# Kernel tuning notes

Hardware: AMD Instinct MI355X
Metric: run time of the kernel (lower is better)

The kernel has to match this reference:

```python
import jax, jax.numpy as jnp
import numpy as np

B, A, NB, BOND = 256, 100, 10, 110
AF, BF, H, DEPTH = 82, 6, 300, 3

def setup_inputs() -> dict:
    key = jax.random.key(0)
    ks = jax.random.split(key, 16)
    atom_feats = jax.random.normal(ks[0], (B, A, AF), dtype=jnp.float32)
    bond_feats = jax.random.normal(ks[1], (B, BOND, BF), dtype=jnp.float32)
    ag_b = jax.random.randint(ks[2], (B, A, NB, 1), 0, B, dtype=jnp.int32)
    ag_a = jax.random.randint(ks[3], (B, A, NB, 1), 0, A, dtype=jnp.int32)
    atom_graph = jnp.concatenate([ag_b, ag_a], axis=-1)
    bg_b = jax.random.randint(ks[4], (B, A, NB, 1), 0, B, dtype=jnp.int32)
    bg_e = jax.random.randint(ks[5], (B, A, NB, 1), 0, BOND, dtype=jnp.int32)
    bond_graph = jnp.concatenate([bg_b, bg_e], axis=-1)
    num_nbs = jax.random.randint(ks[6], (B, A), 0, NB + 1, dtype=jnp.int32)
    n_atoms = jax.random.randint(ks[7], (B,), 50, A + 1, dtype=jnp.int32)
    n_atoms = n_atoms.at[0].set(A)  # padding must equal n_atoms.max()
    sc = lambda i, o: (2.0 / (i + o)) ** 0.5
    w_fc1 = jax.random.normal(ks[8], (AF, H), dtype=jnp.float32) * sc(AF, H)
    w_nei = jax.random.normal(ks[9], (H + BF, H), dtype=jnp.float32) * sc(H + BF, H)
    b_nei = jnp.zeros((H,), dtype=jnp.float32)
    w_atom = jax.random.normal(ks[10], (2 * H, H), dtype=jnp.float32) * sc(2 * H, H)
    b_atom = jnp.zeros((H,), dtype=jnp.float32)
    w2a = jax.random.normal(ks[11], (H, H), dtype=jnp.float32) * sc(H, H)
    w2b = jax.random.normal(ks[12], (BF, H), dtype=jnp.float32) * sc(BF, H)
    w_fc2 = jax.random.normal(ks[13], (H, H), dtype=jnp.float32) * sc(H, H)
    return dict(atom_feats=atom_feats, bond_feats=bond_feats, w_fc1=w_fc1,
                w_nei=w_nei, b_nei=b_nei, w_atom=w_atom, b_atom=b_atom,
                w2a=w2a, w2b=w2b, w_fc2=w_fc2, atom_graph=atom_graph,
                bond_graph=bond_graph, num_nbs=num_nbs, n_atoms=n_atoms)

def reference(atom_feats, bond_feats, w_fc1, w_nei, b_nei, w_atom, b_atom,
              w2a, w2b, w_fc2, atom_graph, bond_graph, num_nbs, n_atoms):
    h = jax.nn.relu(atom_feats @ w_fc1)                      # [B,A,H]
    bondnei = bond_feats[bond_graph[..., 0], bond_graph[..., 1]]  # [B,A,NB,BF]
    mask_neis = (num_nbs[..., None] > jnp.arange(NB, dtype=jnp.int32))[..., None]
    mask_atoms = (n_atoms[:, None] > jnp.arange(A, dtype=jnp.int32))[..., None]
    for i in range(DEPTH):
        atomnei = h[atom_graph[..., 0], atom_graph[..., 1]]  # [B,A,NB,H]
        if i + 1 == DEPTH:
            nei = (atomnei @ w2a) * (bondnei @ w2b)          # [B,A,NB,H]
            nei = jnp.where(mask_neis, nei, 0.0).sum(-2)     # [B,A,H]
            local = (h @ w_fc2) * nei
            local = jnp.where(mask_atoms, local, 0.0)
        else:
            nei = jax.nn.relu(jnp.concatenate([atomnei, bondnei], -1) @ w_nei + b_nei)
            nei = jnp.where(mask_neis, nei, 0.0).sum(-2)
            h = jax.nn.relu(jnp.concatenate([h, nei], -1) @ w_atom + b_atom)
    return local
```

## Files before the change

### kernel.cpp

```cpp
#include <hip/hip_runtime.h>

#define B_    256
#define A_    100
#define NB_   10
#define BOND_ 110
#define AF_   82
#define BF_   6
#define H_    300
#define NP_   320
#define MA_   (B_ * A_)
#define MB_   (B_ * BOND_)
#define KP300 320
#define KP82  96

typedef __attribute__((ext_vector_type(8))) short short8;
typedef __attribute__((ext_vector_type(4))) float f32x4;

__device__ __forceinline__ ushort f2bf(float v) {
    union { float f; unsigned u; } x; x.f = v;
    unsigned r = x.u + 0x7fffu + ((x.u >> 16) & 1u);
    return (ushort)(r >> 16);
}
__device__ __forceinline__ float bf2f(ushort h) {
    union { float f; unsigned u; } x; x.u = ((unsigned)h) << 16;
    return x.f;
}

__device__ __forceinline__ void gload16(const void* g, void* l) {
    __builtin_amdgcn_global_load_lds(
        (const __attribute__((address_space(1))) void*)g,
        (__attribute__((address_space(3))) void*)l, 16, 0, 0);
}

template<bool DUAL, bool BIAS, bool RELU, int OUTMODE>
__global__ __launch_bounds__(256, 2) void mgemm_k(
    const ushort* __restrict__ aH, const ushort* __restrict__ aL,
    const ushort* __restrict__ wH, const ushort* __restrict__ wL,
    const ushort* __restrict__ aH2, const ushort* __restrict__ aL2,
    const ushort* __restrict__ wH2, const ushort* __restrict__ wL2,
    int KP,
    const float* __restrict__ bias,
    const float* __restrict__ E,
    const int*   __restrict__ n_atoms,
    ushort* __restrict__ oHi, ushort* __restrict__ oLo,
    float*  __restrict__ oF)
{
    __shared__ ushort lds[3840 * 8];
    const int tid  = threadIdx.x;
    const int m0   = blockIdx.x * 64;
    const int lane = tid & 63;
    const int l16  = lane & 15;
    const int kg   = lane >> 4;
    const int w    = tid >> 6;

    int sel[15]; int off[15];
    #pragma unroll
    for (int q = 0; q < 15; ++q) {
        int G = q * 256 + tid;
        int s, local;
        if      (G < 320)  { s = 0; local = G; }
        else if (G < 640)  { s = 1; local = G - 320; }
        else if (G < 2240) { s = 2; local = G - 640; }
        else               { s = 3; local = G - 2240; }
        int rc = local / 5;
        int ch = local % 5; if (ch == 4) ch = 3;
        int rowterm = (s < 2) ? (m0 + rc) : rc;
        sel[q] = s;
        off[q] = rowterm * KP * 2 + ch * 16;
    }
    char* ldst = (char*)&lds[0] + ((tid & 192) << 4);

    f32x4 acc[4][5] = {};
    const int aoff = l16 * 80 + kg * 16;
    const int boff = (w * 80 + l16) * 80 + kg * 16;

    const int npass = DUAL ? 2 : 1;
    for (int pass = 0; pass < npass; ++pass) {
        const ushort* s0 = (DUAL && pass) ? aH2 : aH;
        const ushort* s1 = (DUAL && pass) ? aL2 : aL;
        const ushort* s2 = (DUAL && pass) ? wH2 : wH;
        const ushort* s3 = (DUAL && pass) ? wL2 : wL;
        const char* ptr[15];
        #pragma unroll
        for (int q = 0; q < 15; ++q) {
            const ushort* b = (sel[q] == 0) ? s0 : (sel[q] == 1) ? s1 : (sel[q] == 2) ? s2 : s3;
            ptr[q] = (const char*)b + off[q];
        }
        const int ksteps = KP >> 5;
        for (int ks = 0; ks < ksteps; ++ks) {
            __syncthreads();
            #pragma unroll
            for (int q = 0; q < 15; ++q) gload16(ptr[q], ldst + q * 4096);
            __syncthreads();

            short8 ah[4], al[4];
            #pragma unroll
            for (int rt = 0; rt < 4; ++rt) {
                ah[rt] = *(const short8*)((const char*)lds +     0 + aoff + rt * 1280);
                al[rt] = *(const short8*)((const char*)lds +  5120 + aoff + rt * 1280);
            }
            #pragma unroll
            for (int c = 0; c < 5; ++c) {
                short8 bh = *(const short8*)((const char*)lds + 10240 + boff + c * 1280);
                short8 bl = *(const short8*)((const char*)lds + 35840 + boff + c * 1280);
                #pragma unroll
                for (int rt = 0; rt < 4; ++rt) {
                    acc[rt][c] = __builtin_amdgcn_mfma_f32_16x16x32_bf16(ah[rt], bh, acc[rt][c], 0, 0, 0);
                    acc[rt][c] = __builtin_amdgcn_mfma_f32_16x16x32_bf16(al[rt], bh, acc[rt][c], 0, 0, 0);
                    acc[rt][c] = __builtin_amdgcn_mfma_f32_16x16x32_bf16(ah[rt], bl, acc[rt][c], 0, 0, 0);
                }
            }
            #pragma unroll
            for (int q = 0; q < 15; ++q) ptr[q] += 64;
        }
    }

    float biasv[5];
    #pragma unroll
    for (int c = 0; c < 5; ++c) {
        int col = w * 80 + c * 16 + l16;
        biasv[c] = (BIAS && col < H_) ? bias[col] : 0.f;
    }
    #pragma unroll
    for (int rt = 0; rt < 4; ++rt) {
        #pragma unroll
        for (int c = 0; c < 5; ++c) {
            const int col = w * 80 + c * 16 + l16;
            #pragma unroll
            for (int r = 0; r < 4; ++r) {
                const int row = m0 + rt * 16 + kg * 4 + r;
                float v = acc[rt][c][r];
                if (BIAS) v += biasv[c];
                if (RELU) v = fmaxf(v, 0.f);
                if (OUTMODE == 0) {
                    ushort hi = f2bf(v);
                    ushort lo = f2bf(v - bf2f(hi));
                    size_t o = (size_t)row * NP_ + col;
                    oHi[o] = hi; oLo[o] = lo;
                } else if (OUTMODE == 1) {
                    oF[(size_t)row * NP_ + col] = v;
                } else {
                    if (col < H_) {
                        v *= E[(size_t)row * NP_ + col];
                        int b = row / A_;
                        int a = row - b * A_;
                        if (a >= n_atoms[b]) v = 0.f;
                        oF[(size_t)row * H_ + col] = v;
                    }
                }
            }
        }
    }
}

__global__ __launch_bounds__(256) void conv_w_k(
    const float* __restrict__ src, int K, int KP,
    ushort* __restrict__ dhi, ushort* __restrict__ dlo)
{
    int idx = blockIdx.x * 256 + threadIdx.x;
    if (idx >= NP_ * KP) return;
    int c = idx / KP, k = idx - c * KP;
    float v = (c < H_ && k < K) ? src[(size_t)k * H_ + c] : 0.f;
    ushort hi = f2bf(v);
    dhi[idx] = hi;
    dlo[idx] = f2bf(v - bf2f(hi));
}

__global__ __launch_bounds__(256) void conv_af_k(
    const float* __restrict__ src, ushort* __restrict__ dhi, ushort* __restrict__ dlo)
{
    int idx = blockIdx.x * 256 + threadIdx.x;
    if (idx >= MA_ * KP82) return;
    int row = idx / KP82, k = idx - row * KP82;
    float v = (k < AF_) ? src[(size_t)row * AF_ + k] : 0.f;
    ushort hi = f2bf(v);
    dhi[idx] = hi;
    dlo[idx] = f2bf(v - bf2f(hi));
}

__global__ __launch_bounds__(256) void bondmm_k(
    const float* __restrict__ bf, const float* __restrict__ wmat,
    const float* __restrict__ bias, float* __restrict__ out)
{
    int idx = blockIdx.x * 256 + threadIdx.x;
    if (idx >= MB_ * 80) return;
    int row = idx / 80, c4 = idx - row * 80;
    float4 s = make_float4(0.f, 0.f, 0.f, 0.f);
    if (c4 < 75) {
        int col = c4 * 4;
        if (bias) s = *(const float4*)(bias + col);
        #pragma unroll
        for (int k = 0; k < 6; ++k) {
            float b = bf[(size_t)row * 6 + k];
            float4 wv = *(const float4*)(wmat + (size_t)k * H_ + col);
            s.x = fmaf(b, wv.x, s.x); s.y = fmaf(b, wv.y, s.y);
            s.z = fmaf(b, wv.z, s.z); s.w = fmaf(b, wv.w, s.w);
        }
    }
    *(float4*)(out + (size_t)row * NP_ + c4 * 4) = s;
}

__global__ __launch_bounds__(256) void agg_relu_k(
    const float* __restrict__ hw, const float* __restrict__ bwn,
    const int* __restrict__ ag, const int* __restrict__ bg,
    const int* __restrict__ num_nbs,
    ushort* __restrict__ neiH, ushort* __restrict__ neiL)
{
    int idx = blockIdx.x * 256 + threadIdx.x;
    if (idx >= MA_ * 80) return;
    int ba = idx / 80, c4 = idx - ba * 80;
    int nn = num_nbs[ba];
    const int* agp = ag + (size_t)ba * NB_ * 2;
    const int* bgp = bg + (size_t)ba * NB_ * 2;
    float4 s = make_float4(0.f, 0.f, 0.f, 0.f);
    for (int n = 0; n < nn; ++n) {
        int arow = agp[2*n] * A_    + agp[2*n+1];
        int brow = bgp[2*n] * BOND_ + bgp[2*n+1];
        float4 hv = *(const float4*)(hw  + (size_t)arow * NP_ + c4 * 4);
        float4 bv = *(const float4*)(bwn + (size_t)brow * NP_ + c4 * 4);
        s.x += fmaxf(hv.x + bv.x, 0.f); s.y += fmaxf(hv.y + bv.y, 0.f);
        s.z += fmaxf(hv.z + bv.z, 0.f); s.w += fmaxf(hv.w + bv.w, 0.f);
    }
    size_t o = (size_t)ba * NP_ + c4 * 4;
    ushort4 hi, lo;
    hi.x = f2bf(s.x); lo.x = f2bf(s.x - bf2f(hi.x));
    hi.y = f2bf(s.y); lo.y = f2bf(s.y - bf2f(hi.y));
    hi.z = f2bf(s.z); lo.z = f2bf(s.z - bf2f(hi.z));
    hi.w = f2bf(s.w); lo.w = f2bf(s.w - bf2f(hi.w));
    *(ushort4*)(neiH + o) = hi;
    *(ushort4*)(neiL + o) = lo;
}

__global__ __launch_bounds__(256) void agg_prod_k(
    const float* __restrict__ hw2, const float* __restrict__ bw2,
    const int* __restrict__ ag, const int* __restrict__ bg,
    const int* __restrict__ num_nbs, float* __restrict__ neiF)
{
    int idx = blockIdx.x * 256 + threadIdx.x;
    if (idx >= MA_ * 80) return;
    int ba = idx / 80, c4 = idx - ba * 80;
    int nn = num_nbs[ba];
    const int* agp = ag + (size_t)ba * NB_ * 2;
    const int* bgp = bg + (size_t)ba * NB_ * 2;
    float4 s = make_float4(0.f, 0.f, 0.f, 0.f);
    for (int n = 0; n < nn; ++n) {
        int arow = agp[2*n] * A_    + agp[2*n+1];
        int brow = bgp[2*n] * BOND_ + bgp[2*n+1];
        float4 hv = *(const float4*)(hw2 + (size_t)arow * NP_ + c4 * 4);
        float4 bv = *(const float4*)(bw2 + (size_t)brow * NP_ + c4 * 4);
        s.x = fmaf(hv.x, bv.x, s.x); s.y = fmaf(hv.y, bv.y, s.y);
        s.z = fmaf(hv.z, bv.z, s.z); s.w = fmaf(hv.w, bv.w, s.w);
    }
    *(float4*)(neiF + (size_t)ba * NP_ + c4 * 4) = s;
}

extern "C" void kernel_launch(void* const* d_in, const int* in_sizes, int n_in,
                              void* d_out, int out_size, void* d_ws, size_t ws_size,
                              hipStream_t stream)
{
    const float* atom_feats = (const float*)d_in[0];
    const float* bond_feats = (const float*)d_in[1];
    const float* w_fc1      = (const float*)d_in[2];
    const float* w_nei      = (const float*)d_in[3];
    const float* b_nei      = (const float*)d_in[4];
    const float* w_atom     = (const float*)d_in[5];
    const float* b_atom     = (const float*)d_in[6];
    const float* w2a        = (const float*)d_in[7];
    const float* w2b        = (const float*)d_in[8];
    const float* w_fc2      = (const float*)d_in[9];
    const int*   atom_graph = (const int*)d_in[10];
    const int*   bond_graph = (const int*)d_in[11];
    const int*   num_nbs    = (const int*)d_in[12];
    const int*   n_atoms    = (const int*)d_in[13];
    float* out = (float*)d_out;
    (void)in_sizes; (void)n_in; (void)out_size; (void)ws_size;

    const size_t SZ_H16 = (size_t)MA_ * NP_ * 2;
    const size_t SZ_HF  = (size_t)MA_ * NP_ * 4;
    const size_t SZ_BWN = (size_t)MB_ * NP_ * 4;
    const size_t SZ_AF  = (size_t)MA_ * KP82 * 2;
    const size_t SZ_WT  = (size_t)NP_ * KP300 * 2;
    const size_t SZ_WT1 = (size_t)NP_ * KP82 * 2;
    char* p = (char*)d_ws;
    ushort* hA_h = (ushort*)p; p += SZ_H16;
    ushort* hA_l = (ushort*)p; p += SZ_H16;
    ushort* hB_h = (ushort*)p; p += SZ_H16;
    ushort* hB_l = (ushort*)p; p += SZ_H16;
    ushort* nei_h = (ushort*)p; p += SZ_H16;
    ushort* nei_l = (ushort*)p; p += SZ_H16;
    float* hwF = (float*)p; p += SZ_HF;
    float* bwn = (float*)p; p += SZ_BWN;
    ushort* af_h = (ushort*)p; p += SZ_AF;
    ushort* af_l = (ushort*)p; p += SZ_AF;
    ushort* wfc1_h = (ushort*)p; p += SZ_WT1;
    ushort* wfc1_l = (ushort*)p; p += SZ_WT1;
    ushort* wn1_h  = (ushort*)p; p += SZ_WT;
    ushort* wn1_l  = (ushort*)p; p += SZ_WT;
    ushort* wa1_h  = (ushort*)p; p += SZ_WT;
    ushort* wa1_l  = (ushort*)p; p += SZ_WT;
    ushort* wa2_h  = (ushort*)p; p += SZ_WT;
    ushort* wa2_l  = (ushort*)p; p += SZ_WT;
    ushort* w2a_h  = (ushort*)p; p += SZ_WT;
    ushort* w2a_l  = (ushort*)p; p += SZ_WT;
    ushort* wfc2_h = (ushort*)p; p += SZ_WT;
    ushort* wfc2_l = (ushort*)p; p += SZ_WT;
    float* neiF = (float*)hB_h;

    const dim3 blk(256);
    const dim3 gG(MA_ / 64);
    const int  aggG  = (MA_ * 80 + 255) / 256;
    const int  bondG = (MB_ * 80 + 255) / 256;

    conv_af_k<<<(MA_*KP82+255)/256, blk, 0, stream>>>(atom_feats, af_h, af_l);
    conv_w_k<<<(NP_*KP82 +255)/256, blk, 0, stream>>>(w_fc1, AF_, KP82, wfc1_h, wfc1_l);
    conv_w_k<<<(NP_*KP300+255)/256, blk, 0, stream>>>(w_nei,              H_, KP300, wn1_h, wn1_l);
    conv_w_k<<<(NP_*KP300+255)/256, blk, 0, stream>>>(w_atom,             H_, KP300, wa1_h, wa1_l);
    conv_w_k<<<(NP_*KP300+255)/256, blk, 0, stream>>>(w_atom + (size_t)H_*H_, H_, KP300, wa2_h, wa2_l);
    conv_w_k<<<(NP_*KP300+255)/256, blk, 0, stream>>>(w2a,                H_, KP300, w2a_h, w2a_l);
    conv_w_k<<<(NP_*KP300+255)/256, blk, 0, stream>>>(w_fc2,              H_, KP300, wfc2_h, wfc2_l);

    bondmm_k<<<bondG, blk, 0, stream>>>(bond_feats, w_nei + (size_t)H_*H_, b_nei, bwn);

    mgemm_k<false,false,true,0><<<gG, blk, 0, stream>>>(
        af_h, af_l, wfc1_h, wfc1_l, nullptr,nullptr,nullptr,nullptr, KP82,
        nullptr, nullptr, nullptr, hA_h, hA_l, nullptr);

    ushort* hc_h = hA_h; ushort* hc_l = hA_l;
    ushort* hn_h = hB_h; ushort* hn_l = hB_l;
    for (int it = 0; it < 2; ++it) {
        mgemm_k<false,false,false,1><<<gG, blk, 0, stream>>>(
            hc_h, hc_l, wn1_h, wn1_l, nullptr,nullptr,nullptr,nullptr, KP300,
            nullptr, nullptr, nullptr, nullptr, nullptr, hwF);
        agg_relu_k<<<aggG, blk, 0, stream>>>(hwF, bwn, atom_graph, bond_graph, num_nbs, nei_h, nei_l);
        mgemm_k<true,true,true,0><<<gG, blk, 0, stream>>>(
            hc_h, hc_l, wa1_h, wa1_l, nei_h, nei_l, wa2_h, wa2_l, KP300,
            b_atom, nullptr, nullptr, hn_h, hn_l, nullptr);
        ushort* t;
        t = hc_h; hc_h = hn_h; hn_h = t;
        t = hc_l; hc_l = hn_l; hn_l = t;
    }

    bondmm_k<<<bondG, blk, 0, stream>>>(bond_feats, w2b, nullptr, bwn);
    mgemm_k<false,false,false,1><<<gG, blk, 0, stream>>>(
        hc_h, hc_l, w2a_h, w2a_l, nullptr,nullptr,nullptr,nullptr, KP300,
        nullptr, nullptr, nullptr, nullptr, nullptr, hwF);
    agg_prod_k<<<aggG, blk, 0, stream>>>(hwF, bwn, atom_graph, bond_graph, num_nbs, neiF);
    mgemm_k<false,false,false,2><<<gG, blk, 0, stream>>>(
        hc_h, hc_l, wfc2_h, wfc2_l, nullptr,nullptr,nullptr,nullptr, KP300,
        nullptr, neiF, n_atoms, nullptr, nullptr, out);
}
```

Before: 500.4 us.

## Stream pre-fragmented weights from global and triple-buffer activation tiles in GEMM

The GEMM kernel no longer stages weights through LDS. Weights are pre-converted into MFMA fragment order and loaded directly into registers. Activation tiles for the next k-step are prefetched into a three-slot LDS ring, with a vmcnt wait in place of double syncthreads. Each block now covers one molecule (100 rows, 7 row tiles) over a 256-block grid, which raises per-block work and register pressure and drops occupancy to one block per CU.

After: 529.5 us. +5.8%, slower.

```diff
diff --git a/kernel.cpp b/kernel.cpp
--- a/kernel.cpp
+++ b/kernel.cpp
@@ -33,11 +33,11 @@
 }
 
 template<bool DUAL, bool BIAS, bool RELU, int OUTMODE>
-__global__ __launch_bounds__(256, 2) void mgemm_k(
+__global__ __launch_bounds__(256, 1) void mgemm_k(
     const ushort* __restrict__ aH, const ushort* __restrict__ aL,
-    const ushort* __restrict__ wH, const ushort* __restrict__ wL,
+    const ushort* __restrict__ fH, const ushort* __restrict__ fL,
     const ushort* __restrict__ aH2, const ushort* __restrict__ aL2,
-    const ushort* __restrict__ wH2, const ushort* __restrict__ wL2,
+    const ushort* __restrict__ fH2, const ushort* __restrict__ fL2,
     int KP,
     const float* __restrict__ bias,
     const float* __restrict__ E,
@@ -45,74 +45,80 @@
     ushort* __restrict__ oHi, ushort* __restrict__ oLo,
     float*  __restrict__ oF)
 {
-    __shared__ ushort lds[3840 * 8];
+    __shared__ char lds[3 * 20480];
     const int tid  = threadIdx.x;
-    const int m0   = blockIdx.x * 64;
     const int lane = tid & 63;
     const int l16  = lane & 15;
     const int kg   = lane >> 4;
     const int w    = tid >> 6;
-
-    int sel[15]; int off[15];
+    const int rowbase = blockIdx.x * 100;
+
+    const int nks   = KP >> 5;
+    const int total = (DUAL ? 2 : 1) * nks;
+
+    int st_row[5], st_choff[5], st_plane[5];
     #pragma unroll
-    for (int q = 0; q < 15; ++q) {
-        int G = q * 256 + tid;
-        int s, local;
-        if      (G < 320)  { s = 0; local = G; }
-        else if (G < 640)  { s = 1; local = G - 320; }
-        else if (G < 2240) { s = 2; local = G - 640; }
-        else               { s = 3; local = G - 2240; }
-        int rc = local / 5;
-        int ch = local % 5; if (ch == 4) ch = 3;
-        int rowterm = (s < 2) ? (m0 + rc) : rc;
-        sel[q] = s;
-        off[q] = rowterm * KP * 2 + ch * 16;
-    }
-    char* ldst = (char*)&lds[0] + ((tid & 192) << 4);
-
-    f32x4 acc[4][5] = {};
-    const int aoff = l16 * 80 + kg * 16;
-    const int boff = (w * 80 + l16) * 80 + kg * 16;
-
-    const int npass = DUAL ? 2 : 1;
-    for (int pass = 0; pass < npass; ++pass) {
-        const ushort* s0 = (DUAL && pass) ? aH2 : aH;
-        const ushort* s1 = (DUAL && pass) ? aL2 : aL;
-        const ushort* s2 = (DUAL && pass) ? wH2 : wH;
-        const ushort* s3 = (DUAL && pass) ? wL2 : wL;
-        const char* ptr[15];
+    for (int q = 0; q < 5; ++q) {
+        int g = q * 256 + tid;
+        int plane = (g >= 640) ? 1 : 0;
+        int local = g - plane * 640;
+        int row = local / 5;
+        int ch  = local % 5; if (ch == 4) ch = 3;
+        int grow = rowbase + row; if (grow >= MA_) grow = MA_ - 1;
+        st_row[q] = grow; st_choff[q] = ch * 16; st_plane[q] = plane;
+    }
+
+    auto stage = [&](int t) {
+        int pass = (DUAL && t >= nks) ? 1 : 0;
+        int ks   = t - (pass ? nks : 0);
+        const ushort* SH = pass ? aH2 : aH;
+        const ushort* SL = pass ? aL2 : aL;
+        char* dst = (char*)lds + (t % 3) * 20480 + (tid & 192) * 16;
         #pragma unroll
-        for (int q = 0; q < 15; ++q) {
-            const ushort* b = (sel[q] == 0) ? s0 : (sel[q] == 1) ? s1 : (sel[q] == 2) ? s2 : s3;
-            ptr[q] = (const char*)b + off[q];
-        }
-        const int ksteps = KP >> 5;
-        for (int ks = 0; ks < ksteps; ++ks) {
-            __syncthreads();
-            #pragma unroll
-            for (int q = 0; q < 15; ++q) gload16(ptr[q], ldst + q * 4096);
-            __syncthreads();
-
-            short8 ah[4], al[4];
-            #pragma unroll
-            for (int rt = 0; rt < 4; ++rt) {
-                ah[rt] = *(const short8*)((const char*)lds +     0 + aoff + rt * 1280);
-                al[rt] = *(const short8*)((const char*)lds +  5120 + aoff + rt * 1280);
-            }
+        for (int q = 0; q < 5; ++q) {
+            const ushort* src = (st_plane[q] ? SL : SH) + (size_t)st_row[q] * KP + ks * 32;
+            gload16((const char*)src + st_choff[q], dst + q * 4096);
+        }
+    };
+
+    f32x4 acc[7][5] = {};
+
+    stage(0);
+    for (int tk = 0; tk < total; ++tk) {
+        short8 bh[5], bl[5];
+        {
+            int pass = (DUAL && tk >= nks) ? 1 : 0;
+            int ks   = tk - (pass ? nks : 0);
+            const ushort* FHp = pass ? fH2 : fH;
+            const ushort* FLp = pass ? fL2 : fL;
+            size_t base = ((size_t)ks * 20 + w * 5) * 512 + (size_t)lane * 8;
             #pragma unroll
             for (int c = 0; c < 5; ++c) {
-                short8 bh = *(const short8*)((const char*)lds + 10240 + boff + c * 1280);
-                short8 bl = *(const short8*)((const char*)lds + 35840 + boff + c * 1280);
-                #pragma unroll
-                for (int rt = 0; rt < 4; ++rt) {
-                    acc[rt][c] = __builtin_amdgcn_mfma_f32_16x16x32_bf16(ah[rt], bh, acc[rt][c], 0, 0, 0);
-                    acc[rt][c] = __builtin_amdgcn_mfma_f32_16x16x32_bf16(al[rt], bh, acc[rt][c], 0, 0, 0);
-                    acc[rt][c] = __builtin_amdgcn_mfma_f32_16x16x32_bf16(ah[rt], bl, acc[rt][c], 0, 0, 0);
-                }
+                bh[c] = *(const short8*)(FHp + base + c * 512);
+                bl[c] = *(const short8*)(FLp + base + c * 512);
             }
+        }
+        if (tk + 1 < total) stage(tk + 1);
+
+        if (tk + 1 < total) { asm volatile("s_waitcnt vmcnt(5)" ::: "memory"); }
+        else                { asm volatile("s_waitcnt vmcnt(0)" ::: "memory"); }
+        __builtin_amdgcn_s_barrier();
+        __builtin_amdgcn_sched_barrier(0);
+
+        const char* ab = (const char*)lds + (tk % 3) * 20480;
+        const int ao = l16 * 80 + kg * 16;
+        #pragma unroll
+        for (int rt = 0; rt < 7; ++rt) {
+            short8 ah = *(const short8*)(ab + rt * 1280 + ao);
+            short8 al = *(const short8*)(ab + 10240 + rt * 1280 + ao);
             #pragma unroll
-            for (int q = 0; q < 15; ++q) ptr[q] += 64;
-        }
+            for (int c = 0; c < 5; ++c) {
+                acc[rt][c] = __builtin_amdgcn_mfma_f32_16x16x32_bf16(ah, bh[c], acc[rt][c], 0, 0, 0);
+                acc[rt][c] = __builtin_amdgcn_mfma_f32_16x16x32_bf16(al, bh[c], acc[rt][c], 0, 0, 0);
+                acc[rt][c] = __builtin_amdgcn_mfma_f32_16x16x32_bf16(ah, bl[c], acc[rt][c], 0, 0, 0);
+            }
+        }
+        __builtin_amdgcn_s_barrier();
     }
 
     float biasv[5];
@@ -122,13 +128,15 @@
         biasv[c] = (BIAS && col < H_) ? bias[col] : 0.f;
     }
     #pragma unroll
-    for (int rt = 0; rt < 4; ++rt) {
+    for (int rt = 0; rt < 7; ++rt) {
         #pragma unroll
         for (int c = 0; c < 5; ++c) {
             const int col = w * 80 + c * 16 + l16;
             #pragma unroll
             for (int r = 0; r < 4; ++r) {
-                const int row = m0 + rt * 16 + kg * 4 + r;
+                const int lrow = rt * 16 + kg * 4 + r;
+                if (lrow >= 100) continue;
+                const int row = rowbase + lrow;
                 float v = acc[rt][c][r];
                 if (BIAS) v += biasv[c];
                 if (RELU) v = fmaxf(v, 0.f);
@@ -153,17 +161,30 @@
     }
 }
 
-__global__ __launch_bounds__(256) void conv_w_k(
+__global__ __launch_bounds__(256) void conv_wfrag_k(
     const float* __restrict__ src, int K, int KP,
-    ushort* __restrict__ dhi, ushort* __restrict__ dlo)
-{
-    int idx = blockIdx.x * 256 + threadIdx.x;
-    if (idx >= NP_ * KP) return;
-    int c = idx / KP, k = idx - c * KP;
-    float v = (c < H_ && k < K) ? src[(size_t)k * H_ + c] : 0.f;
-    ushort hi = f2bf(v);
-    dhi[idx] = hi;
-    dlo[idx] = f2bf(v - bf2f(hi));
+    ushort* __restrict__ dH, ushort* __restrict__ dL)
+{
+    int idx = blockIdx.x * 256 + threadIdx.x;
+    int nwords = (KP >> 5) * 20 * 64;
+    if (idx >= nwords) return;
+    int lane = idx & 63;
+    int t  = idx >> 6;
+    int ct = t % 20;
+    int ks = t / 20;
+    int col = ct * 16 + (lane & 15);
+    int k0  = ks * 32 + (lane >> 4) * 8;
+    short8 hv, lv;
+    #pragma unroll
+    for (int j = 0; j < 8; ++j) {
+        int k = k0 + j;
+        float v = (col < H_ && k < K) ? src[(size_t)k * H_ + col] : 0.f;
+        ushort h = f2bf(v);
+        hv[j] = (short)h;
+        lv[j] = (short)f2bf(v - bf2f(h));
+    }
+    *(short8*)(dH + (size_t)idx * 8) = hv;
+    *(short8*)(dL + (size_t)idx * 8) = lv;
 }
 
 __global__ __launch_bounds__(256) void conv_af_k(
@@ -307,17 +328,19 @@
     float* neiF = (float*)hB_h;
 
     const dim3 blk(256);
-    const dim3 gG(MA_ / 64);
+    const dim3 gG(256);
     const int  aggG  = (MA_ * 80 + 255) / 256;
     const int  bondG = (MB_ * 80 + 255) / 256;
+    const int  fw300 = ((KP300 >> 5) * 20 * 64 + 255) / 256;
+    const int  fw96  = ((KP82  >> 5) * 20 * 64 + 255) / 256;
 
     conv_af_k<<<(MA_*KP82+255)/256, blk, 0, stream>>>(atom_feats, af_h, af_l);
-    conv_w_k<<<(NP_*KP82 +255)/256, blk, 0, stream>>>(w_fc1, AF_, KP82, wfc1_h, wfc1_l);
-    conv_w_k<<<(NP_*KP300+255)/256, blk, 0, stream>>>(w_nei,              H_, KP300, wn1_h, wn1_l);
-    conv_w_k<<<(NP_*KP300+255)/256, blk, 0, stream>>>(w_atom,             H_, KP300, wa1_h, wa1_l);
-    conv_w_k<<<(NP_*KP300+255)/256, blk, 0, stream>>>(w_atom + (size_t)H_*H_, H_, KP300, wa2_h, wa2_l);
-    conv_w_k<<<(NP_*KP300+255)/256, blk, 0, stream>>>(w2a,                H_, KP300, w2a_h, w2a_l);
-    conv_w_k<<<(NP_*KP300+255)/256, blk, 0, stream>>>(w_fc2,              H_, KP300, wfc2_h, wfc2_l);
+    conv_wfrag_k<<<fw96,  blk, 0, stream>>>(w_fc1, AF_, KP82, wfc1_h, wfc1_l);
+    conv_wfrag_k<<<fw300, blk, 0, stream>>>(w_nei,                 H_, KP300, wn1_h, wn1_l);
+    conv_wfrag_k<<<fw300, blk, 0, stream>>>(w_atom,                H_, KP300, wa1_h, wa1_l);
+    conv_wfrag_k<<<fw300, blk, 0, stream>>>(w_atom + (size_t)H_*H_, H_, KP300, wa2_h, wa2_l);
+    conv_wfrag_k<<<fw300, blk, 0, stream>>>(w2a,                   H_, KP300, w2a_h, w2a_l);
+    conv_wfrag_k<<<fw300, blk, 0, stream>>>(w_fc2,                 H_, KP300, wfc2_h, wfc2_l);
 
     bondmm_k<<<bondG, blk, 0, stream>>>(bond_feats, w_nei + (size_t)H_*H_, b_nei, bwn);
 
```
